# Kernel tuning notes

Hardware: AMD Instinct MI355X
Metric: run time of the kernel (lower is better)

The kernel has to match this reference:

```python
import jax, jax.numpy as jnp
import numpy as np

EMBED = 768
FFN = 3072
HEADS = 12
HEAD_DIM = EMBED // HEADS
B, T = 4, 2048


def _layer_norm(x, g, b, eps=1e-5):
    m = jnp.mean(x, axis=-1, keepdims=True)
    v = jnp.mean((x - m) ** 2, axis=-1, keepdims=True)
    return (x - m) * jax.lax.rsqrt(v + eps) * g + b


def setup_inputs() -> dict:
    key = jax.random.key(0)
    ks = jax.random.split(key, 8)
    s_e = 1.0 / np.sqrt(EMBED)
    s_f = 1.0 / np.sqrt(FFN)
    # weights stored [in, out] (transpose of torch Linear layout)
    return {
        "x": jax.random.normal(ks[0], (B, T, EMBED), dtype=jnp.float32),
        "ln1_g": jnp.ones((EMBED,), jnp.float32),
        "ln1_b": jnp.zeros((EMBED,), jnp.float32),
        "wq": jax.random.uniform(ks[1], (EMBED, EMBED), jnp.float32, -s_e, s_e),
        "bq": jnp.zeros((EMBED,), jnp.float32),
        "wk": jax.random.uniform(ks[2], (EMBED, EMBED), jnp.float32, -s_e, s_e),
        "bk": jnp.zeros((EMBED,), jnp.float32),
        "wv": jax.random.uniform(ks[3], (EMBED, EMBED), jnp.float32, -s_e, s_e),
        "bv": jnp.zeros((EMBED,), jnp.float32),
        "wo": jax.random.uniform(ks[4], (EMBED, EMBED), jnp.float32, -s_e, s_e),
        "bo": jnp.zeros((EMBED,), jnp.float32),
        "ln2_g": jnp.ones((EMBED,), jnp.float32),
        "ln2_b": jnp.zeros((EMBED,), jnp.float32),
        "w1": jax.random.uniform(ks[5], (EMBED, FFN), jnp.float32, -s_e, s_e),
        "b1": jnp.zeros((FFN,), jnp.float32),
        "w2": jax.random.uniform(ks[6], (FFN, EMBED), jnp.float32, -s_f, s_f),
        "b2": jnp.zeros((EMBED,), jnp.float32),
    }


def reference(x, ln1_g, ln1_b, wq, bq, wk, bk, wv, bv, wo, bo,
              ln2_g, ln2_b, w1, b1, w2, b2):
    Bx, Tx, C = x.shape
    # --- self-attention block (pre-norm) ---
    residual = x
    h = _layer_norm(x, ln1_g, ln1_b)
    q = (h @ wq + bq).reshape(Bx, Tx, HEADS, HEAD_DIM)
    k = (h @ wk + bk).reshape(Bx, Tx, HEADS, HEAD_DIM)
    v = (h @ wv + bv).reshape(Bx, Tx, HEADS, HEAD_DIM)
    scale = 1.0 / np.sqrt(HEAD_DIM)
    attn = jnp.einsum('bqhd,bkhd->bhqk', q, k) * scale  # [B,H,T,T]
    attn = jax.nn.softmax(attn, axis=-1)
    o = jnp.einsum('bhqk,bkhd->bqhd', attn, v).reshape(Bx, Tx, C)
    x = residual + (o @ wo + bo)
    # --- FFN block (pre-norm) ---
    residual = x
    h = _layer_norm(x, ln2_g, ln2_b)
    h = jax.nn.gelu(h @ w1 + b1, approximate=False)
    x = residual + (h @ w2 + b2)
    return x
```

## Files before the change

### kernel.cpp

```cpp
#include <hip/hip_runtime.h>
#include <hip/hip_bf16.h>

#define EMBED 768
#define FFNDIM 3072
#define HEADS 12
#define HDIM  64
#define BB    4
#define TT    2048
#define MTOK  (BB*TT)

typedef __hip_bfloat16 bf16;
typedef __attribute__((ext_vector_type(8))) short short8;
typedef __attribute__((ext_vector_type(4))) float f32x4;
typedef __attribute__((ext_vector_type(16))) float f32x16;
typedef __attribute__((ext_vector_type(4))) unsigned short ushort4v;

__device__ __forceinline__ f32x4 mfma16(short8 a, short8 b, f32x4 c) {
  return __builtin_amdgcn_mfma_f32_16x16x32_bf16(a, b, c, 0, 0, 0);
}
__device__ __forceinline__ f32x16 mfma32(short8 a, short8 b, f32x16 c) {
  return __builtin_amdgcn_mfma_f32_32x32x16_bf16(a, b, c, 0, 0, 0);
}

__device__ __forceinline__ unsigned short f2bf(float f) {
  union { float f; unsigned int u; } v; v.f = f;
  unsigned int u = v.u;
  return (unsigned short)((u + 0x7fffu + ((u >> 16) & 1u)) >> 16);
}

__device__ __forceinline__ float fexp2(float x) {
#if __has_builtin(__builtin_amdgcn_exp2f)
  return __builtin_amdgcn_exp2f(x);
#else
  return exp2f(x);
#endif
}

__device__ __forceinline__ float gelu_f(float v) {
  const float ax = fabsf(v) * 0.70710678118f;
  const float t = __builtin_amdgcn_rcpf(1.f + 0.3275911f * ax);
  float p = 1.061405429f;
  p = p * t - 1.453152027f;
  p = p * t + 1.421413741f;
  p = p * t - 0.284496736f;
  p = p * t + 0.254829592f;
  p = p * t;
  const float e = fexp2(-ax * ax * 1.4426950408889634f);
  float er = 1.f - p * e;
  er = (v < 0.f) ? -er : er;
  return 0.5f * v * (1.f + er);
}

__device__ __forceinline__ unsigned cvtpk(float lo, float hi) {
  unsigned r;
  asm("v_cvt_pk_bf16_f32 %0, %1, %2" : "=v"(r) : "v"(lo), "v"(hi));
  return r;
}
__device__ __forceinline__ void pl32swap(unsigned& vdst, unsigned& vsrc) {
  asm("v_permlane32_swap_b32 %0, %1" : "+v"(vdst), "+v"(vsrc));
}

__device__ __forceinline__ void gl_lds16(const void* g, void* l) {
  __builtin_amdgcn_global_load_lds((const __attribute__((address_space(1))) void*)g,
                                   (__attribute__((address_space(3))) void*)l, 16, 0, 0);
}

template <int N>
__device__ __forceinline__ void wait_vm() {
  asm volatile("s_waitcnt vmcnt(%0)" :: "i"(N) : "memory");
  __builtin_amdgcn_sched_barrier(0);
}
__device__ __forceinline__ void block_barrier() {
  __builtin_amdgcn_sched_barrier(0);
  __builtin_amdgcn_s_barrier();
  __builtin_amdgcn_sched_barrier(0);
}

#define QSCALE 0.18033688011112042f
#define DEFER_THR 11.54f


struct TArgs {
  const float* src[6];
  bf16* dst[6];
  int K[6];
  int N[6];
};

__global__ __launch_bounds__(256) void transpose_k(TArgs ta) {
  const int mi = blockIdx.z;
  const int K = ta.K[mi], N = ta.N[mi];
  const int nt = N / 32;
  const int bx = blockIdx.x % nt, by = blockIdx.x / nt;
  const int n0 = bx * 32, k0 = by * 32;
  if (k0 >= K) return;
  __shared__ float t[32][33];
  const float* __restrict__ W = ta.src[mi];
  bf16* __restrict__ Wt = ta.dst[mi];
  const int tx = threadIdx.x & 31, ty = threadIdx.x >> 5;
#pragma unroll
  for (int i = 0; i < 4; ++i) {
    int kk = ty + i * 8;
    t[tx][kk] = W[(size_t)(k0 + kk) * N + n0 + tx];
  }
  __syncthreads();
#pragma unroll
  for (int i = 0; i < 4; ++i) {
    int nn = ty + i * 8;
    Wt[(size_t)(n0 + nn) * K + k0 + tx] = __float2bfloat16(t[nn][tx]);
  }
}

__global__ __launch_bounds__(256) void ln_k(const float* __restrict__ x,
                                            const float* __restrict__ g,
                                            const float* __restrict__ b,
                                            bf16* __restrict__ out) {
  const int row = blockIdx.x * 4 + (threadIdx.x >> 6);
  const int lane = threadIdx.x & 63;
  const float* xr = x + (size_t)row * EMBED;
  float4 v[3];
  float s = 0.f;
#pragma unroll
  for (int i = 0; i < 3; ++i) {
    v[i] = *(const float4*)&xr[i * 256 + lane * 4];
    s += v[i].x + v[i].y + v[i].z + v[i].w;
  }
#pragma unroll
  for (int m = 1; m < 64; m <<= 1) s += __shfl_xor(s, m);
  const float mean = s * (1.f / 768.f);
  float ss = 0.f;
#pragma unroll
  for (int i = 0; i < 3; ++i) {
    float dx = v[i].x - mean, dy = v[i].y - mean, dz = v[i].z - mean, dw = v[i].w - mean;
    ss += dx * dx + dy * dy + dz * dz + dw * dw;
  }
#pragma unroll
  for (int m = 1; m < 64; m <<= 1) ss += __shfl_xor(ss, m);
  const float rstd = rsqrtf(ss * (1.f / 768.f) + 1e-5f);
#pragma unroll
  for (int i = 0; i < 3; ++i) {
    float4 g4 = *(const float4*)&g[i * 256 + lane * 4];
    float4 b4 = *(const float4*)&b[i * 256 + lane * 4];
    ushort4v o4;
    o4[0] = f2bf((v[i].x - mean) * rstd * g4.x + b4.x);
    o4[1] = f2bf((v[i].y - mean) * rstd * g4.y + b4.y);
    o4[2] = f2bf((v[i].z - mean) * rstd * g4.z + b4.z);
    o4[3] = f2bf((v[i].w - mean) * rstd * g4.w + b4.w);
    *(ushort4v*)&out[(size_t)row * EMBED + i * 256 + lane * 4] = o4;
  }
}

template <int EPI, int TN>
__global__ __launch_bounds__(256) void gemm_bt_k(
    const bf16* __restrict__ A, const bf16* __restrict__ Bt,
    const float* __restrict__ bias, const float* __restrict__ bias2,
    const float* __restrict__ bias3, const float* __restrict__ resid,
    float* __restrict__ outf, bf16* __restrict__ outb,
    bf16* __restrict__ outk, bf16* __restrict__ outvt,
    int N, int K) {
  constexpr int MI = (TN == 128) ? 4 : 2;
  constexpr int SN = (TN == 128) ? 4 : 3;
  constexpr int ABUF = 128 * 32;
  constexpr int BBUF = TN * 32;
  __shared__ __align__(16) bf16 smem[3 * ABUF + 3 * BBUF];
  bf16* Al = smem;
  bf16* Bl = smem + 3 * ABUF;

  const int tid = threadIdx.x;
  const int lane = tid & 63;
  const int w = tid >> 6;
  const int l16 = lane & 15, g = lane >> 4;
  const int wrbase = (TN == 128) ? (w >> 1) * 64 : w * 32;
  const int wcbase = (TN == 128) ? (w & 1) * 64 : 0;

  const int nbx = N / TN;
  const int logical = ((int)blockIdx.x & 7) * ((int)gridDim.x >> 3) + ((int)blockIdx.x >> 3);
  const int m0 = (logical / nbx) * 128, n0 = (logical % nbx) * TN;

  f32x4 acc[MI][4];
#pragma unroll
  for (int i = 0; i < MI; ++i)
#pragma unroll
    for (int j = 0; j < 4; ++j) acc[i][j] = {0.f, 0.f, 0.f, 0.f};

  const int st_r = lane >> 2;
  const int st_c = ((lane & 3) ^ ((lane >> 3) & 3)) * 8;
  const size_t a_base = (size_t)(m0 + w * 32) * K;
  const size_t b_base = (TN == 128) ? (size_t)(n0 + w * 32) * K
                                    : (size_t)(n0 + w * 16) * K;

  auto stage = [&](int bufi, int kt) {
#pragma unroll
    for (int p = 0; p < 2; ++p)
      gl_lds16(A + a_base + (size_t)(p * 16 + st_r) * K + kt + st_c,
               &Al[bufi * ABUF + (w * 32 + p * 16) * 32]);
    if constexpr (TN == 128) {
#pragma unroll
      for (int p = 0; p < 2; ++p)
        gl_lds16(Bt + b_base + (size_t)(p * 16 + st_r) * K + kt + st_c,
                 &Bl[bufi * BBUF + (w * 32 + p * 16) * 32]);
    } else {
      gl_lds16(Bt + b_base + (size_t)st_r * K + kt + st_c, &Bl[bufi * BBUF + (w * 16) * 32]);
    }
  };

  const int nt = K >> 5;
  stage(0, 0);
  stage(1, 32);
  const int sw = (l16 >> 1) & 3;
  int buf = 0;
  for (int t = 0; t < nt; ++t) {
    if (t < nt - 1) wait_vm<SN>(); else wait_vm<0>();
    block_barrier();
    if (t + 2 < nt) {
      int nb = buf + 2; if (nb >= 3) nb -= 3;
      stage(nb, (t + 2) * 32);
    }
    short8 af[MI], bfr[4];
#pragma unroll
    for (int i = 0; i < MI; ++i)
      af[i] = *(const short8*)&Al[buf * ABUF + (wrbase + i * 16 + l16) * 32 + (g ^ sw) * 8];
#pragma unroll
    for (int j = 0; j < 4; ++j)
      bfr[j] = *(const short8*)&Bl[buf * BBUF + (wcbase + j * 16 + l16) * 32 + (g ^ sw) * 8];
#pragma unroll
    for (int i = 0; i < MI; ++i)
#pragma unroll
      for (int j = 0; j < 4; ++j) acc[i][j] = mfma16(af[i], bfr[j], acc[i][j]);
    buf = (buf == 2) ? 0 : buf + 1;
  }

  const int crow = m0 + wrbase + g * 4;
  const int ccol = n0 + wcbase + l16;

  if constexpr (EPI == 0) {
    const int region = n0 / EMBED;
    const float* bp = (region == 0) ? bias : (region == 1) ? bias2 : bias3;
    const int bb2 = m0 >> 11;
    const int kb0 = (m0 & 2047) >> 5;
    if (region < 2) {
      const float sc = (region == 0) ? QSCALE : 1.0f;
      bf16* __restrict__ fb = (region == 0) ? outb : outk;
      __syncthreads();
      bf16* S = smem;
#pragma unroll
      for (int j = 0; j < 4; ++j) {
        const int cn = ccol - region * EMBED + j * 16;
        const float bvv = bp[cn];
        const int nl = wcbase + j * 16 + l16;
#pragma unroll
        for (int i = 0; i < MI; ++i)
#pragma unroll
          for (int rr = 0; rr < 4; ++rr) {
            const int mlcl = wrbase + i * 16 + g * 4 + rr;
            S[mlcl * 128 + (nl ^ ((mlcl & 15) << 3))] =
                __float2bfloat16((acc[i][j][rr] + bvv) * sc);
          }
      }
      __syncthreads();
      const int hbase = (n0 - region * EMBED) >> 6;
#pragma unroll
      for (int gg = 0; gg < 8; ++gg) {
        const int rid = gg * 256 + tid;
        const int hp = rid >> 10;
        const int rest2 = rid & 1023;
        const int kbc = rest2 >> 6;
        const int kbl = kbc >> 2, c = kbc & 3;
        const int lid = rest2 & 63;
        const int hl = lid >> 5, l32r = lid & 31;
        const int m_l = kbl * 32 + l32r;
        const int nl = hp * 64 + c * 16 + hl * 8;
        short8 vv = *(const short8*)&S[m_l * 128 + (nl ^ ((m_l & 15) << 3))];
        const size_t fidx =
            ((((size_t)(bb2 * HEADS + hbase + hp) * 64 + kb0 + kbl) * 4 + c) * 64 +
             lid) * 8;
        *(short8*)&fb[fidx] = vv;
      }
    } else {
      __syncthreads();
      constexpr int SP = 136;
      bf16* S = smem;
#pragma unroll
      for (int j = 0; j < 4; ++j) {
        const int cn = ccol - 2 * EMBED + j * 16;
        const float bvv = bp[cn];
        const int nl = wcbase + j * 16 + l16;
#pragma unroll
        for (int i = 0; i < MI; ++i) {
          ushort4v pk;
#pragma unroll
          for (int rr = 0; rr < 4; ++rr) pk[rr] = f2bf(acc[i][j][rr] + bvv);
          *(ushort4v*)&S[nl * SP + wrbase + i * 16 + g * 4] = pk;
        }
      }
      __syncthreads();
      const int hbase = (n0 - 2 * EMBED) >> 6;
#pragma unroll
      for (int gg = 0; gg < 8; ++gg) {
        const int rid = gg * 256 + tid;
        const int hp = rid >> 10;
        const int rest2 = rid & 1023;
        const int kbl = rest2 >> 8;
        const int ks = (rest2 >> 7) & 1;
        const int dc = (rest2 >> 6) & 1;
        const int hl = (rest2 >> 5) & 1;
        const int l32r = rest2 & 31;
        const int nl = hp * 64 + dc * 32 + l32r;
        const int m_l = kbl * 32 + ks * 16 + hl * 8;
        short8 vv = *(const short8*)&S[nl * SP + m_l];
        const size_t fidx =
            ((((size_t)(bb2 * HEADS + hbase + hp) * 64 + kb0 + kbl) * 8 + ks * 4 +
              dc * 2 + hl) * 32 + l32r) * 8;
        *(short8*)&outvt[fidx] = vv;
      }
    }
  } else if constexpr (EPI == 1) {
    constexpr int SW = TN + 4;
    float* S32 = (float*)smem;
    const int mychunk = w >> 1;
#pragma unroll
    for (int c = 0; c < 2; ++c) {
      __syncthreads();
      if (mychunk == c) {
        const int rbase = wrbase - c * 64;
#pragma unroll
        for (int j = 0; j < 4; ++j) {
          const int nl = wcbase + j * 16 + l16;
          const float bvv = bias[n0 + nl];
#pragma unroll
          for (int i = 0; i < MI; ++i)
#pragma unroll
            for (int rr = 0; rr < 4; ++rr)
              S32[(rbase + i * 16 + g * 4 + rr) * SW + nl] = acc[i][j][rr] + bvv;
        }
      }
      __syncthreads();
      if constexpr (TN == 128) {
#pragma unroll
        for (int p = 0; p < 8; ++p) {
          const int rowc = p * 8 + (tid >> 5);
          const int c4 = (tid & 31) * 4;
          const int m = m0 + c * 64 + rowc;
          float4 rv = *(const float4*)&resid[(size_t)m * N + n0 + c4];
          const float* sp = &S32[rowc * SW + c4];
          float4 ov;
          ov.x = rv.x + sp[0]; ov.y = rv.y + sp[1];
          ov.z = rv.z + sp[2]; ov.w = rv.w + sp[3];
          *(float4*)&outf[(size_t)m * N + n0 + c4] = ov;
        }
      } else {
#pragma unroll
        for (int p = 0; p < 4; ++p) {
          const int rowc = p * 16 + (tid >> 4);
          const int c4 = (tid & 15) * 4;
          const int m = m0 + c * 64 + rowc;
          float4 rv = *(const float4*)&resid[(size_t)m * N + n0 + c4];
          const float* sp = &S32[rowc * SW + c4];
          float4 ov;
          ov.x = rv.x + sp[0]; ov.y = rv.y + sp[1];
          ov.z = rv.z + sp[2]; ov.w = rv.w + sp[3];
          *(float4*)&outf[(size_t)m * N + n0 + c4] = ov;
        }
      }
    }
  } else {
    __syncthreads();
    bf16* S = smem;
#pragma unroll
    for (int j = 0; j < 4; ++j) {
      const int cn = ccol + j * 16;
      const float bvv = bias[cn];
      const int nl = wcbase + j * 16 + l16;
#pragma unroll
      for (int i = 0; i < MI; ++i)
#pragma unroll
        for (int rr = 0; rr < 4; ++rr) {
          const int mlcl = wrbase + i * 16 + g * 4 + rr;
          S[mlcl * 128 + (nl ^ ((mlcl & 15) << 3))] =
              __float2bfloat16(gelu_f(acc[i][j][rr] + bvv));
        }
    }
    __syncthreads();
#pragma unroll
    for (int pp = 0; pp < 8; ++pp) {
      const int m_l = pp * 16 + (tid >> 4);
      const int c = tid & 15;
      short8 vv = *(const short8*)&S[m_l * 128 + ((c ^ (m_l & 15)) << 3)];
      *(short8*)&outb[(size_t)(m0 + m_l) * N + n0 + c * 8] = vv;
    }
  }
}

__global__ __launch_bounds__(256, 4) void flash11_k(const bf16* __restrict__ qfb,
                                                    const bf16* __restrict__ kfb,
                                                    const bf16* __restrict__ vfb,
                                                    bf16* __restrict__ po,
                                                    float2* __restrict__ ml) {
  const int tid = threadIdx.x, lane = tid & 63;
  const int l32 = lane & 31, hl = lane >> 5;
  const int w = tid >> 6;
  const int logical = ((int)blockIdx.x & 7) * 192 + ((int)blockIdx.x >> 3);
  const int qt = logical & 15;
  const int rest = logical >> 4;
  const int half = rest & 1;
  const int hb = rest >> 1;
  const int h = hb % HEADS, b = hb / HEADS;
  const int qbi = qt * 4 + w;
  const int kv0 = half * (TT / 2);
  const size_t bh = (size_t)(b * HEADS + h);

  short8 qf[4];
  {
    const bf16* qp = qfb + ((bh * 64 + qbi) * 4) * 512 + lane * 8;
#pragma unroll
    for (int c = 0; c < 4; ++c) qf[c] = *(const short8*)&qp[c * 512];
  }
  const bf16* __restrict__ kbb = kfb + bh * 64 * 2048;
  const bf16* __restrict__ vbb = vfb + bh * 64 * 2048;

  f32x16 oacc0, oacc1;
#pragma unroll
  for (int i = 0; i < 16; ++i) { oacc0[i] = 0.f; oacc1[i] = 0.f; }
  float mrun = -1.0e30f, lrun = 0.f;

  auto subtile = [&](int kvabs) {
    const int kb = kvabs >> 5;
    const bf16* kp = kbb + (size_t)kb * 2048 + lane * 8;
    short8 kf[4];
#pragma unroll
    for (int c = 0; c < 4; ++c) kf[c] = *(const short8*)&kp[c * 512];

    f32x16 s;
#pragma unroll
    for (int i = 0; i < 16; ++i) s[i] = 0.f;
    __builtin_amdgcn_s_setprio(1);
#pragma unroll
    for (int c = 0; c < 4; ++c) s = mfma32(kf[c], qf[c], s);
    __builtin_amdgcn_s_setprio(0);

    float m0 = fmaxf(fmaxf(s[0], s[1]), s[2]);
    float m1 = fmaxf(fmaxf(s[3], s[4]), s[5]);
    float m2 = fmaxf(fmaxf(s[6], s[7]), s[8]);
    float m3 = fmaxf(fmaxf(s[9], s[10]), s[11]);
    float m4 = fmaxf(fmaxf(s[12], s[13]), s[14]);
    float mx = fmaxf(fmaxf(fmaxf(m0, m1), fmaxf(m2, m3)), fmaxf(m4, s[15]));
    mx = fmaxf(mx, __shfl_xor(mx, 32));

    if (!__all(mx <= mrun + DEFER_THR)) {
      const float mn = fmaxf(mrun, mx);
      const float al = fexp2(mrun - mn);
      lrun *= al;
#pragma unroll
      for (int i = 0; i < 16; ++i) { oacc0[i] *= al; oacc1[i] *= al; }
      mrun = mn;
    }

#pragma unroll
    for (int i = 0; i < 16; ++i) s[i] = fexp2(s[i] - mrun);
    float a8[8];
#pragma unroll
    for (int i = 0; i < 8; ++i) a8[i] = s[2 * i] + s[2 * i + 1];
    float ps = ((a8[0] + a8[1]) + (a8[2] + a8[3])) + ((a8[4] + a8[5]) + (a8[6] + a8[7]));
    ps += __shfl_xor(ps, 32);
    lrun += ps;

    union { unsigned u[4]; short8 s8; } pa0, pa1;
    {
      unsigned U = cvtpk(s[0], s[1]), V = cvtpk(s[4], s[5]);
      pl32swap(V, U); pa0.u[0] = U; pa0.u[2] = V;
      unsigned U1 = cvtpk(s[2], s[3]), V1 = cvtpk(s[6], s[7]);
      pl32swap(V1, U1); pa0.u[1] = U1; pa0.u[3] = V1;
    }
    {
      unsigned U = cvtpk(s[8], s[9]), V = cvtpk(s[12], s[13]);
      pl32swap(V, U); pa1.u[0] = U; pa1.u[2] = V;
      unsigned U1 = cvtpk(s[10], s[11]), V1 = cvtpk(s[14], s[15]);
      pl32swap(V1, U1); pa1.u[1] = U1; pa1.u[3] = V1;
    }

    const bf16* vp = vbb + (size_t)kb * 2048 + lane * 8;
    short8 vf[4];
#pragma unroll
    for (int ks = 0; ks < 2; ++ks)
#pragma unroll
      for (int dc = 0; dc < 2; ++dc)
        vf[ks * 2 + dc] = *(const short8*)&vp[(ks * 4 + dc * 2) * 256];

    __builtin_amdgcn_s_setprio(1);
    oacc0 = mfma32(vf[0], pa0.s8, oacc0);
    oacc0 = mfma32(vf[2], pa1.s8, oacc0);
    oacc1 = mfma32(vf[1], pa0.s8, oacc1);
    oacc1 = mfma32(vf[3], pa1.s8, oacc1);
    __builtin_amdgcn_s_setprio(0);
  };

  const int NT = (TT / 2) / 64;
  for (int t = 0; t < NT; ++t) {
    const int base = kv0 + t * 64;
    subtile(base);
    subtile(base + 32);
  }

  const int q0 = qbi * 32;
  bf16* pp = po + ((size_t)((half * BB + b) * HEADS + h) * TT + q0 + l32) * 64;
#pragma unroll
  for (int a = 0; a < 4; ++a) {
    ushort4v pk4;
#pragma unroll
    for (int bb = 0; bb < 4; ++bb) pk4[bb] = f2bf(oacc0[a * 4 + bb]);
    *(ushort4v*)&pp[a * 8 + hl * 4] = pk4;
#pragma unroll
    for (int bb = 0; bb < 4; ++bb) pk4[bb] = f2bf(oacc1[a * 4 + bb]);
    *(ushort4v*)&pp[32 + a * 8 + hl * 4] = pk4;
  }
  if (hl == 0) {
    float2 v2; v2.x = mrun; v2.y = lrun;
    ml[(size_t)((half * BB + b) * HEADS + h) * TT + q0 + l32] = v2;
  }
}

__global__ __launch_bounds__(256) void combine_k(const bf16* __restrict__ po,
                                                 const float2* __restrict__ ml,
                                                 bf16* __restrict__ o) {
  const int row = blockIdx.x * 4 + (threadIdx.x >> 6);
  const int lane = threadIdx.x & 63;
  const size_t NR = (size_t)BB * HEADS * TT;
  const float2 a = ml[row];
  const float2 c = ml[NR + row];
  const float M = fmaxf(a.x, c.x);
  const float w0 = fexp2(a.x - M), w1 = fexp2(c.x - M);
  const float inv = 1.f / (w0 * a.y + w1 * c.y);
  const float o0 = __bfloat162float(po[(size_t)row * 64 + lane]);
  const float o1 = __bfloat162float(po[NR * 64 + (size_t)row * 64 + lane]);
  const float val = (w0 * o0 + w1 * o1) * inv;
  const int b = row / (HEADS * TT);
  const int rem = row % (HEADS * TT);
  const int h = rem / TT, t = rem % TT;
  o[((size_t)(b * TT + t)) * EMBED + h * HDIM + lane] = __float2bfloat16(val);
}

extern "C" void kernel_launch(void* const* d_in, const int* in_sizes, int n_in,
                              void* d_out, int out_size, void* d_ws,
                              size_t ws_size, hipStream_t stream) {
  const float* x = (const float*)d_in[0];
  const float* ln1g = (const float*)d_in[1];
  const float* ln1b = (const float*)d_in[2];
  const float* wq = (const float*)d_in[3];
  const float* bq = (const float*)d_in[4];
  const float* wk = (const float*)d_in[5];
  const float* bk = (const float*)d_in[6];
  const float* wv = (const float*)d_in[7];
  const float* bv = (const float*)d_in[8];
  const float* wo = (const float*)d_in[9];
  const float* bo = (const float*)d_in[10];
  const float* ln2g = (const float*)d_in[11];
  const float* ln2b = (const float*)d_in[12];
  const float* w1 = (const float*)d_in[13];
  const float* b1 = (const float*)d_in[14];
  const float* w2 = (const float*)d_in[15];
  const float* b2 = (const float*)d_in[16];
  float* out = (float*)d_out;

  char* ws = (char*)d_ws;
  size_t off = 0;
  auto alloc = [&](size_t bytes) {
    char* p = ws + off;
    off += (bytes + 255) & ~(size_t)255;
    return p;
  };
  bf16* wqkv_t = (bf16*)alloc((size_t)2304 * 768 * 2);
  bf16* wo_t = (bf16*)alloc((size_t)768 * 768 * 2);
  bf16* w1_t = (bf16*)alloc((size_t)3072 * 768 * 2);
  bf16* w2_t = (bf16*)alloc((size_t)768 * 3072 * 2);
  bf16* h = (bf16*)alloc((size_t)MTOK * EMBED * 2);
  char* qkvo = alloc((size_t)MTOK * EMBED * 2 * 4);
  bf16* qb = (bf16*)qkvo;
  bf16* kb = qb + (size_t)MTOK * EMBED;
  bf16* vtb = kb + (size_t)MTOK * EMBED;
  bf16* ob = vtb + (size_t)MTOK * EMBED;
  bf16* h1 = (bf16*)qkvo;
  float* x1 = (float*)alloc((size_t)MTOK * EMBED * 4);
  (void)ws_size;
  bf16* po = (bf16*)x1;
  float2* mlb = (float2*)h;

  TArgs ta;
  ta.src[0] = wq; ta.dst[0] = wqkv_t;                  ta.K[0] = 768;  ta.N[0] = 768;
  ta.src[1] = wk; ta.dst[1] = wqkv_t + 768 * 768;      ta.K[1] = 768;  ta.N[1] = 768;
  ta.src[2] = wv; ta.dst[2] = wqkv_t + 2 * 768 * 768;  ta.K[2] = 768;  ta.N[2] = 768;
  ta.src[3] = wo; ta.dst[3] = wo_t;                    ta.K[3] = 768;  ta.N[3] = 768;
  ta.src[4] = w1; ta.dst[4] = w1_t;                    ta.K[4] = 768;  ta.N[4] = 3072;
  ta.src[5] = w2; ta.dst[5] = w2_t;                    ta.K[5] = 3072; ta.N[5] = 768;

  transpose_k<<<dim3(2304, 1, 6), dim3(256), 0, stream>>>(ta);
  ln_k<<<dim3(MTOK / 4), dim3(256), 0, stream>>>(x, ln1g, ln1b, h);
  gemm_bt_k<0, 128><<<dim3((2304 / 128) * (MTOK / 128)), dim3(256), 0, stream>>>(
      h, wqkv_t, bq, bk, bv, nullptr, nullptr, qb, kb, vtb, 2304, 768);
  flash11_k<<<dim3(16 * HEADS * BB * 2), dim3(256), 0, stream>>>(qb, kb, vtb, po, mlb);
  combine_k<<<dim3(BB * HEADS * TT / 4), dim3(256), 0, stream>>>(po, mlb, ob);
  gemm_bt_k<1, 64><<<dim3((768 / 64) * (MTOK / 128)), dim3(256), 0, stream>>>(
      ob, wo_t, bo, nullptr, nullptr, x, x1, nullptr, nullptr, nullptr, 768, 768);
  ln_k<<<dim3(MTOK / 4), dim3(256), 0, stream>>>(x1, ln2g, ln2b, h);
  gemm_bt_k<2, 128><<<dim3((3072 / 128) * (MTOK / 128)), dim3(256), 0, stream>>>(
      h, w1_t, b1, nullptr, nullptr, nullptr, nullptr, h1, nullptr, nullptr, 3072, 768);
  gemm_bt_k<1, 128><<<dim3((768 / 128) * (MTOK / 128)), dim3(256), 0, stream>>>(
      h1, w2_t, b2, nullptr, nullptr, x1, out, nullptr, nullptr, nullptr, 768, 3072);
}
```

Baseline: 289.5 us.

## Remove split-KV attention and combine kernel; normalize in flash kernel

The flash attention kernel now processes all 64 KV tiles per query block instead of splitting the KV range in two halves. It normalizes by the running sum itself and writes the final head output directly into the token-major buffer. This removes the separate combine kernel and the round trip of partial outputs and max/sum statistics through memory. The cost is halving the number of blocks launched, which may leave compute units underoccupied and lengthen each block's serial KV loop.

Result: faster. 276.2 us (-4.6%).

```diff
diff --git a/kernel.cpp b/kernel.cpp
--- a/kernel.cpp
+++ b/kernel.cpp
@@ -391,22 +391,18 @@
   }
 }
 
-__global__ __launch_bounds__(256, 4) void flash11_k(const bf16* __restrict__ qfb,
+__global__ __launch_bounds__(256, 4) void flash13_k(const bf16* __restrict__ qfb,
                                                     const bf16* __restrict__ kfb,
                                                     const bf16* __restrict__ vfb,
-                                                    bf16* __restrict__ po,
-                                                    float2* __restrict__ ml) {
+                                                    bf16* __restrict__ o) {
   const int tid = threadIdx.x, lane = tid & 63;
   const int l32 = lane & 31, hl = lane >> 5;
   const int w = tid >> 6;
-  const int logical = ((int)blockIdx.x & 7) * 192 + ((int)blockIdx.x >> 3);
+  const int logical = ((int)blockIdx.x & 7) * 96 + ((int)blockIdx.x >> 3);
   const int qt = logical & 15;
-  const int rest = logical >> 4;
-  const int half = rest & 1;
-  const int hb = rest >> 1;
+  const int hb = logical >> 4;
   const int h = hb % HEADS, b = hb / HEADS;
   const int qbi = qt * 4 + w;
-  const int kv0 = half * (TT / 2);
   const size_t bh = (size_t)(b * HEADS + h);
 
   short8 qf[4];
@@ -423,8 +419,7 @@
   for (int i = 0; i < 16; ++i) { oacc0[i] = 0.f; oacc1[i] = 0.f; }
   float mrun = -1.0e30f, lrun = 0.f;
 
-  auto subtile = [&](int kvabs) {
-    const int kb = kvabs >> 5;
+  auto subtile = [&](int kb) {
     const bf16* kp = kbb + (size_t)kb * 2048 + lane * 8;
     short8 kf[4];
 #pragma unroll
@@ -494,49 +489,21 @@
     __builtin_amdgcn_s_setprio(0);
   };
 
-  const int NT = (TT / 2) / 64;
-  for (int t = 0; t < NT; ++t) {
-    const int base = kv0 + t * 64;
-    subtile(base);
-    subtile(base + 32);
-  }
-
+  for (int kb = 0; kb < 64; ++kb) subtile(kb);
+
+  const float inv = 1.f / lrun;
   const int q0 = qbi * 32;
-  bf16* pp = po + ((size_t)((half * BB + b) * HEADS + h) * TT + q0 + l32) * 64;
+  bf16* op = o + (size_t)(b * TT + q0 + l32) * EMBED + h * HDIM;
 #pragma unroll
   for (int a = 0; a < 4; ++a) {
     ushort4v pk4;
 #pragma unroll
-    for (int bb = 0; bb < 4; ++bb) pk4[bb] = f2bf(oacc0[a * 4 + bb]);
-    *(ushort4v*)&pp[a * 8 + hl * 4] = pk4;
-#pragma unroll
-    for (int bb = 0; bb < 4; ++bb) pk4[bb] = f2bf(oacc1[a * 4 + bb]);
-    *(ushort4v*)&pp[32 + a * 8 + hl * 4] = pk4;
-  }
-  if (hl == 0) {
-    float2 v2; v2.x = mrun; v2.y = lrun;
-    ml[(size_t)((half * BB + b) * HEADS + h) * TT + q0 + l32] = v2;
-  }
-}
-
-__global__ __launch_bounds__(256) void combine_k(const bf16* __restrict__ po,
-                                                 const float2* __restrict__ ml,
-                                                 bf16* __restrict__ o) {
-  const int row = blockIdx.x * 4 + (threadIdx.x >> 6);
-  const int lane = threadIdx.x & 63;
-  const size_t NR = (size_t)BB * HEADS * TT;
-  const float2 a = ml[row];
-  const float2 c = ml[NR + row];
-  const float M = fmaxf(a.x, c.x);
-  const float w0 = fexp2(a.x - M), w1 = fexp2(c.x - M);
-  const float inv = 1.f / (w0 * a.y + w1 * c.y);
-  const float o0 = __bfloat162float(po[(size_t)row * 64 + lane]);
-  const float o1 = __bfloat162float(po[NR * 64 + (size_t)row * 64 + lane]);
-  const float val = (w0 * o0 + w1 * o1) * inv;
-  const int b = row / (HEADS * TT);
-  const int rem = row % (HEADS * TT);
-  const int h = rem / TT, t = rem % TT;
-  o[((size_t)(b * TT + t)) * EMBED + h * HDIM + lane] = __float2bfloat16(val);
+    for (int bb = 0; bb < 4; ++bb) pk4[bb] = f2bf(oacc0[a * 4 + bb] * inv);
+    *(ushort4v*)&op[a * 8 + hl * 4] = pk4;
+#pragma unroll
+    for (int bb = 0; bb < 4; ++bb) pk4[bb] = f2bf(oacc1[a * 4 + bb] * inv);
+    *(ushort4v*)&op[32 + a * 8 + hl * 4] = pk4;
+  }
 }
 
 extern "C" void kernel_launch(void* const* d_in, const int* in_sizes, int n_in,
@@ -581,8 +548,6 @@
   bf16* h1 = (bf16*)qkvo;
   float* x1 = (float*)alloc((size_t)MTOK * EMBED * 4);
   (void)ws_size;
-  bf16* po = (bf16*)x1;
-  float2* mlb = (float2*)h;
 
   TArgs ta;
   ta.src[0] = wq; ta.dst[0] = wqkv_t;                  ta.K[0] = 768;  ta.N[0] = 768;
@@ -596,8 +561,7 @@
   ln_k<<<dim3(MTOK / 4), dim3(256), 0, stream>>>(x, ln1g, ln1b, h);
   gemm_bt_k<0, 128><<<dim3((2304 / 128) * (MTOK / 128)), dim3(256), 0, stream>>>(
       h, wqkv_t, bq, bk, bv, nullptr, nullptr, qb, kb, vtb, 2304, 768);
-  flash11_k<<<dim3(16 * HEADS * BB * 2), dim3(256), 0, stream>>>(qb, kb, vtb, po, mlb);
-  combine_k<<<dim3(BB * HEADS * TT / 4), dim3(256), 0, stream>>>(po, mlb, ob);
+  flash13_k<<<dim3(16 * HEADS * BB), dim3(256), 0, stream>>>(qb, kb, vtb, ob);
   gemm_bt_k<1, 64><<<dim3((768 / 64) * (MTOK / 128)), dim3(256), 0, stream>>>(
       ob, wo_t, bo, nullptr, nullptr, x, x1, nullptr, nullptr, nullptr, 768, 768);
   ln_k<<<dim3(MTOK / 4), dim3(256), 0, stream>>>(x1, ln2g, ln2b, h);
```
